# Kernel tuning notes

Hardware: AMD Instinct MI355X
Metric: run time of the kernel (lower is better)

## Reference

```python
import jax, jax.numpy as jnp
import numpy as np

NUM_MAIN_SEQ_ATOMS = 12   # backbone atoms per RNA residue
NUM_NEIGHBOUR = 30
EMBEDDING_DIM = 32
EPS = 1e-5
BIG_DIST = 1000000.0


def setup_inputs() -> dict:
    key = jax.random.key(0)
    k1, k2, k3 = jax.random.split(key, 3)
    B, L, A = 2, 256, NUM_MAIN_SEQ_ATOMS
    coords = jax.random.normal(k1, (B, L, A, 3), dtype=jnp.float32) * 10.0
    mask = jax.random.randint(k2, (B, L), 0, 2).astype(jnp.int32)
    emb_table = jax.random.normal(k3, (NUM_MAIN_SEQ_ATOMS, EMBEDDING_DIM), dtype=jnp.float32)
    scale = jnp.ones((1, 1, EMBEDDING_DIM), dtype=jnp.float32)
    shift = jnp.zeros((1, 1, EMBEDDING_DIM), dtype=jnp.float32)
    return {"coords": coords, "mask": mask, "emb_table": emb_table,
            "scale": scale, "shift": shift}


def _graph_norm(features, m, scale, shift):
    # features: (B,N,E); m: (B,N) float {0,1}
    mm = m[:, :, None]                                   # (B,N,1)
    masked = features * mm
    cnt = jnp.maximum(mm.sum(axis=1, keepdims=True), 1.0)  # (B,1,1)
    mean = masked.sum(axis=1, keepdims=True) / cnt
    var = ((masked - mean) ** 2).sum(axis=1, keepdims=True) / cnt
    std = jnp.sqrt(var + EPS)
    out = ((features - mean) / std) * scale + shift
    return out * mm


def reference(coords, mask, emb_table, scale, shift):
    B, L, A, _ = coords.shape
    N = L * A
    atom_coords = coords.reshape(B, N, 3)
    atom_mask = jnp.repeat(mask, A, axis=1)              # (B,N) int
    m = atom_mask.astype(coords.dtype)

    # ---- encoder: cyclic atom-type embedding + graph norm ----
    atom_types = jnp.arange(N) % A                       # (N,)
    emb = emb_table[atom_types][None] * m[:, :, None]    # (B,N,E)
    encode = _graph_norm(emb, m, scale, shift)

    # ---- kNN graph: O(N^2) pairwise distances + masked top-k ----
    d = atom_coords[:, None, :, :] - atom_coords[:, :, None, :]  # (B,N,N,3)
    dist = jnp.sqrt((d ** 2).sum(-1) + 1e-6)             # (B,N,N)
    m2 = m[:, None, :] * m[:, :, None]                   # (B,N,N)
    dist = dist * m2 + (1.0 - m2) * BIG_DIST

    k = min(NUM_NEIGHBOUR, N)
    neg_d, edge_idx = jax.lax.top_k(-dist, k)            # smallest-k
    dist_neighbors = -neg_d                              # (B,N,k)

    pad = (atom_mask == 0)[:, :, None]                   # (B,N,1)
    edge_idx = jnp.where(pad, 0, edge_idx)
    dist_neighbors = jnp.where(pad, BIG_DIST, dist_neighbors)
    return atom_coords, atom_mask, encode, dist_neighbors, edge_idx
```

## Files before the change

### kernel.cpp

```cpp
#include <hip/hip_runtime.h>
#include <math.h>

#define NA   12
#define NL   256
#define NN   3072
#define NB   2
#define ED   32
#define KNB  30
#define BIGD 1000000.0f

#define OFF_COORDS 0
#define OFF_MASK   18432
#define OFF_ENC    24576
#define OFF_DIST   221184
#define OFF_IDX    405504

#define KEYVAL 0xFFFFF000u
#define KEYIDX 0x00000FFFu
#define MASKED_D2 1e12f

static __device__ __forceinline__ unsigned umin32(unsigned a, unsigned b) {
    return a < b ? a : b;
}

#define DPP_MIN_STEP(CTRL)                                                        \
    {                                                                             \
        int t_ = __builtin_amdgcn_update_dpp(v_, v_, (CTRL), 0xf, 0xf, false);    \
        v_ = (int)umin32((unsigned)v_, (unsigned)t_);                             \
    }

#define TREE8(A0,A1,A2,A3,A4,A5,A6,A7) \
    umin32(umin32(umin32((A0),(A1)), umin32((A2),(A3))), \
           umin32(umin32((A4),(A5)), umin32((A6),(A7))))

#define REMOVE_RESCAN(G)                                                          \
    {                                                                             \
        _Pragma("unroll")                                                         \
        for (int u = 0; u < 8; ++u) {                                             \
            const int t = (G) * 8 + u;                                            \
            k[t] = (k[t] == wkey) ? 0xFFFFFFFFu : k[t];                           \
        }                                                                         \
        gm[(G)] = TREE8(k[(G)*8+0],k[(G)*8+1],k[(G)*8+2],k[(G)*8+3],              \
                        k[(G)*8+4],k[(G)*8+5],k[(G)*8+6],k[(G)*8+7]);             \
    }

__global__ __launch_bounds__(512, 4) void fused_kernel(const float* __restrict__ coords,
                                                       const int* __restrict__ mask,
                                                       const float* __restrict__ emb,
                                                       const float* __restrict__ scale,
                                                       const float* __restrict__ shift,
                                                       float* __restrict__ out) {
    __shared__ float4 sc4[NN];

    int tid  = threadIdx.x;
    int lane = tid & 63;
    int wave = tid >> 6;
    int b    = (int)(blockIdx.x) / 192;
    int rblk = (int)(blockIdx.x) - b * 192;
    const float4* cg4 = (const float4*)(coords + (size_t)b * NN * 3);
    const int*    mb  = mask + b * NL;

    for (int task = tid; task < NN / 4; task += 512) {
        float4 f0 = cg4[3 * task + 0];
        float4 f1 = cg4[3 * task + 1];
        float4 f2 = cg4[3 * task + 2];
        int base = 4 * task;
        float m0 = (float)mb[((base + 0) * 43691) >> 19];
        float m1 = (float)mb[((base + 1) * 43691) >> 19];
        float m2 = (float)mb[((base + 2) * 43691) >> 19];
        float m3 = (float)mb[((base + 3) * 43691) >> 19];
        sc4[base + 0] = make_float4(f0.x, f0.y, f0.z, m0);
        sc4[base + 1] = make_float4(f0.w, f1.x, f1.y, m1);
        sc4[base + 2] = make_float4(f1.z, f1.w, f2.x, m2);
        sc4[base + 3] = make_float4(f2.y, f2.z, f2.w, m3);
    }
    __syncthreads();

#pragma unroll 1
    for (int rr = 0; rr < 2; ++rr) {
        int i   = rblk * 16 + wave + rr * 8;
        int row = b * NN + i;
        float4 q = sc4[i];

        if (q.w != 0.f) {
            unsigned k[48];
            unsigned gm[6];

#pragma unroll
            for (int t = 0; t < 48; ++t) {
                int j = t * 64 + lane;
                float4 v = sc4[j];
                float dx = v.x - q.x, dy = v.y - q.y, dz = v.z - q.z;
                float s = dx * dx + dy * dy + dz * dz + 1e-6f;
                s = (v.w != 0.f) ? s : MASKED_D2;
                k[t] = (__float_as_uint(s) & KEYVAL) | (unsigned)j;
            }
#pragma unroll
            for (int g = 0; g < 6; ++g)
                gm[g] = TREE8(k[g*8+0],k[g*8+1],k[g*8+2],k[g*8+3],
                              k[g*8+4],k[g*8+5],k[g*8+6],k[g*8+7]);

            unsigned cur = umin32(umin32(umin32(gm[0], gm[1]), umin32(gm[2], gm[3])),
                                  umin32(gm[4], gm[5]));
            unsigned rkey = 0u;

            for (int it = 0; it < KNB; ++it) {
                int v_ = (int)cur;
                DPP_MIN_STEP(0xB1)
                DPP_MIN_STEP(0x4E)
                DPP_MIN_STEP(0x141)
                DPP_MIN_STEP(0x140)
                unsigned r0  = (unsigned)__builtin_amdgcn_readlane(v_, 0);
                unsigned r16 = (unsigned)__builtin_amdgcn_readlane(v_, 16);
                unsigned r32 = (unsigned)__builtin_amdgcn_readlane(v_, 32);
                unsigned r48 = (unsigned)__builtin_amdgcn_readlane(v_, 48);
                unsigned wkey = umin32(umin32(r0, r16), umin32(r32, r48));
                rkey = (lane == it) ? wkey : rkey;

                int wg = (int)((wkey & KEYIDX) >> 9);
                switch (wg) {
                    case 0: REMOVE_RESCAN(0); break;
                    case 1: REMOVE_RESCAN(1); break;
                    case 2: REMOVE_RESCAN(2); break;
                    case 3: REMOVE_RESCAN(3); break;
                    case 4: REMOVE_RESCAN(4); break;
                    default: REMOVE_RESCAN(5); break;
                }
                cur = umin32(umin32(umin32(gm[0], gm[1]), umin32(gm[2], gm[3])),
                             umin32(gm[4], gm[5]));
            }

            if (lane < KNB) {
                float d2 = __uint_as_float(rkey & KEYVAL);
                out[OFF_DIST + (size_t)row * KNB + lane] = sqrtf(d2);
                out[OFF_IDX  + (size_t)row * KNB + lane] = (float)(rkey & KEYIDX);
            }
        } else {
            if (lane < KNB) {
                out[OFF_DIST + (size_t)row * KNB + lane] = BIGD;
                out[OFF_IDX  + (size_t)row * KNB + lane] = 0.f;
            }
        }
    }

    int gidx = (int)blockIdx.x * 512 + tid;

    {
        const int4* m4 = (const int4*)(mask + b * NL);
        int4 mv = m4[lane];
        float S = (float)(mv.x + mv.y + mv.z + mv.w);
#pragma unroll
        for (int m = 1; m < 64; m <<= 1) S += __shfl_xor(S, m);

        int c = gidx & (ED - 1);
        float colsum = 0.f, sumsq = 0.f;
#pragma unroll
        for (int a = 0; a < NA; ++a) {
            float e = emb[a * ED + c];
            colsum += e; sumsq += e * e;
        }
        float cnt  = fmaxf(12.0f * S, 1.0f);
        float mean = S * colsum / cnt;
        float acc  = sumsq - 2.0f * mean * colsum + 12.0f * mean * mean;
        float var  = (S * acc + ((float)NN - 12.0f * S) * mean * mean) / cnt;
        float rstd = 1.0f / sqrtf(var + 1e-5f);

        int n  = (gidx >> 5) - b * NN;
        int nr = (n * 43691) >> 19;
        float mi = sc4[n].w;
        float v = 0.f;
        if (mi != 0.f) {
            float en = emb[(n - nr * NA) * ED + c];
            v = (en - mean) * rstd * scale[c] + shift[c];
        }
        out[OFF_ENC + gidx] = v;
    }

    if (gidx < NB * NN * 3) {
        out[OFF_COORDS + gidx] = coords[gidx];
    }

    if (gidx < NB * NN) {
        int bb = gidx >= NN ? 1 : 0;
        int nn = gidx - bb * NN;
        int nr = (nn * 43691) >> 19;
        out[OFF_MASK + gidx] = (float)mask[bb * NL + nr];
    }
}

extern "C" void kernel_launch(void* const* d_in, const int* in_sizes, int n_in,
                              void* d_out, int out_size, void* d_ws, size_t ws_size,
                              hipStream_t stream) {
    const float* coords = (const float*)d_in[0];
    const int*   mask   = (const int*)d_in[1];
    const float* emb    = (const float*)d_in[2];
    const float* scale  = (const float*)d_in[3];
    const float* shift  = (const float*)d_in[4];
    float* out = (float*)d_out;

    fused_kernel<<<NB * (NN / 16), 512, 0, stream>>>(coords, mask, emb, scale, shift, out);
}
```

Measured before the change: 102.6 us.

## Halve block size, fold mask into additive distance term, simplify staging

Launches twice as many 256-thread blocks, each handling 8 query rows, and sets launch bounds to (256,3). Each lane now stages coordinates with scalar loads, and the mask is stored as an additive term (1e-6 for valid atoms, 1e12 for masked) so the distance becomes a single fma chain with no select. The aim is better load balance across CUs and fewer ALU ops in the hot distance loop. The cost is that each block still stages the whole 48KB point set into LDS, so total staging traffic doubles, and the scalar global loads are less coalesced.

```diff
diff --git a/kernel.cpp b/kernel.cpp
--- a/kernel.cpp
+++ b/kernel.cpp
@@ -17,7 +17,8 @@
 
 #define KEYVAL 0xFFFFF000u
 #define KEYIDX 0x00000FFFu
-#define MASKED_D2 1e12f
+#define MASKED_ADD 1e12f
+#define VALID_ADD  1e-6f
 
 static __device__ __forceinline__ unsigned umin32(unsigned a, unsigned b) {
     return a < b ? a : b;
@@ -44,7 +45,7 @@
                         k[(G)*8+4],k[(G)*8+5],k[(G)*8+6],k[(G)*8+7]);             \
     }
 
-__global__ __launch_bounds__(512, 4) void fused_kernel(const float* __restrict__ coords,
+__global__ __launch_bounds__(256, 3) void fused_kernel(const float* __restrict__ coords,
                                                        const int* __restrict__ mask,
                                                        const float* __restrict__ emb,
                                                        const float* __restrict__ scale,
@@ -55,34 +56,27 @@
     int tid  = threadIdx.x;
     int lane = tid & 63;
     int wave = tid >> 6;
-    int b    = (int)(blockIdx.x) / 192;
-    int rblk = (int)(blockIdx.x) - b * 192;
-    const float4* cg4 = (const float4*)(coords + (size_t)b * NN * 3);
-    const int*    mb  = mask + b * NL;
+    int b    = (int)(blockIdx.x) / 384;
+    int rblk = (int)(blockIdx.x) - b * 384;
+    const float* cb = coords + (size_t)b * NN * 3;
+    const int*   mb = mask + b * NL;
 
-    for (int task = tid; task < NN / 4; task += 512) {
-        float4 f0 = cg4[3 * task + 0];
-        float4 f1 = cg4[3 * task + 1];
-        float4 f2 = cg4[3 * task + 2];
-        int base = 4 * task;
-        float m0 = (float)mb[((base + 0) * 43691) >> 19];
-        float m1 = (float)mb[((base + 1) * 43691) >> 19];
-        float m2 = (float)mb[((base + 2) * 43691) >> 19];
-        float m3 = (float)mb[((base + 3) * 43691) >> 19];
-        sc4[base + 0] = make_float4(f0.x, f0.y, f0.z, m0);
-        sc4[base + 1] = make_float4(f0.w, f1.x, f1.y, m1);
-        sc4[base + 2] = make_float4(f1.z, f1.w, f2.x, m2);
-        sc4[base + 3] = make_float4(f2.y, f2.z, f2.w, m3);
+#pragma unroll
+    for (int s = 0; s < 12; ++s) {
+        int e = tid + s * 256;
+        int r = (e * 43691) >> 19;
+        float aw = mb[r] ? VALID_ADD : MASKED_ADD;
+        sc4[e] = make_float4(cb[3 * e + 0], cb[3 * e + 1], cb[3 * e + 2], aw);
     }
     __syncthreads();
 
 #pragma unroll 1
     for (int rr = 0; rr < 2; ++rr) {
-        int i   = rblk * 16 + wave + rr * 8;
+        int i   = rblk * 8 + wave * 2 + rr;
         int row = b * NN + i;
         float4 q = sc4[i];
 
-        if (q.w != 0.f) {
+        if (q.w < 1.0f) {
             unsigned k[48];
             unsigned gm[6];
 
@@ -91,8 +85,7 @@
                 int j = t * 64 + lane;
                 float4 v = sc4[j];
                 float dx = v.x - q.x, dy = v.y - q.y, dz = v.z - q.z;
-                float s = dx * dx + dy * dy + dz * dz + 1e-6f;
-                s = (v.w != 0.f) ? s : MASKED_D2;
+                float s = fmaf(dx, dx, fmaf(dy, dy, fmaf(dz, dz, v.w)));
                 k[t] = (__float_as_uint(s) & KEYVAL) | (unsigned)j;
             }
 #pragma unroll
@@ -143,7 +136,7 @@
         }
     }
 
-    int gidx = (int)blockIdx.x * 512 + tid;
+    int gidx = (int)blockIdx.x * 256 + tid;
 
     {
         const int4* m4 = (const int4*)(mask + b * NL);
@@ -167,9 +160,8 @@
 
         int n  = (gidx >> 5) - b * NN;
         int nr = (n * 43691) >> 19;
-        float mi = sc4[n].w;
         float v = 0.f;
-        if (mi != 0.f) {
+        if (sc4[n].w < 1.0f) {
             float en = emb[(n - nr * NA) * ED + c];
             v = (en - mean) * rstd * scale[c] + shift[c];
         }
@@ -198,5 +190,5 @@
     const float* shift  = (const float*)d_in[4];
     float* out = (float*)d_out;
 
-    fused_kernel<<<NB * (NN / 16), 512, 0, stream>>>(coords, mask, emb, scale, shift, out);
+    fused_kernel<<<NB * (NN / 8), 256, 0, stream>>>(coords, mask, emb, scale, shift, out);
 }
```

Result: faster. 93.84 us (-8.6%).
